# Performance work log

Measured on AMD Instinct MI355X. Metric: run time of the kernel, lower is better.

The kernel has to match this reference:

```python
import jax, jax.numpy as jnp
import numpy as np

N, C_IN, C_OUT, T, V, K = 32, 64, 128, 300, 25, 3
EPS = 1e-5


def setup_inputs() -> dict:
    key = jax.random.key(0)
    ks = jax.random.split(key, 10)
    x = jax.random.normal(ks[0], (N, C_IN, T, V), dtype=jnp.float32)
    # fixed adjacency buffer (requires_grad=False in torch) and learned attention mask
    A = jax.random.uniform(ks[1], (K, V, V), dtype=jnp.float32)
    graph_attn = jnp.ones((K, V, V), dtype=jnp.float32)  # nn.init.constant_(1)
    # per-subset 1x1 conv weights/biases, stacked: [K, C_out, C_in]
    Wg = jax.random.normal(ks[2], (K, C_OUT, C_IN), dtype=jnp.float32) * np.sqrt(2.0 / (C_OUT * K))
    bg = jnp.zeros((K, C_OUT), dtype=jnp.float32)
    # main BN affine (torch init: weight=1e-6, bias=0; use small random for a nontrivial test)
    bn_gamma = jax.random.normal(ks[3], (C_OUT,), dtype=jnp.float32) * 0.1 + 1.0
    bn_beta = jax.random.normal(ks[4], (C_OUT,), dtype=jnp.float32) * 0.1
    # residual branch (in != out): 1x1 conv + BN
    Wr = jax.random.normal(ks[5], (C_OUT, C_IN), dtype=jnp.float32) * np.sqrt(2.0 / C_IN)
    br = jnp.zeros((C_OUT,), dtype=jnp.float32)
    rbn_gamma = jax.random.normal(ks[6], (C_OUT,), dtype=jnp.float32) * 0.1 + 1.0
    rbn_beta = jax.random.normal(ks[7], (C_OUT,), dtype=jnp.float32) * 0.1
    return {"x": x, "A": A, "graph_attn": graph_attn, "Wg": Wg, "bg": bg,
            "bn_gamma": bn_gamma, "bn_beta": bn_beta,
            "Wr": Wr, "br": br, "rbn_gamma": rbn_gamma, "rbn_beta": rbn_beta}


def _batchnorm(z, gamma, beta):
    # training-mode BatchNorm2d: biased batch stats over (N, T, V)
    mean = jnp.mean(z, axis=(0, 2, 3), keepdims=True)
    var = jnp.var(z, axis=(0, 2, 3), keepdims=True)
    zhat = (z - mean) * jax.lax.rsqrt(var + EPS)
    return zhat * gamma[None, :, None, None] + beta[None, :, None, None]


def reference(x, A, graph_attn, Wg, bg, bn_gamma, bn_beta, Wr, br, rbn_gamma, rbn_beta):
    Ae = A * graph_attn                                   # [K, V, V]
    # per-subset graph aggregation: (x.view(N, C*T, V) @ Ae[k])  -> [K, N, C, T, V]
    xA = jnp.einsum('nctv,kvw->knctw', x, Ae)
    # per-subset 1x1 conv then sum over subsets; biases sum as well
    hidden = jnp.einsum('knctv,koc->notv', xA, Wg) + jnp.sum(bg, axis=0)[None, :, None, None]
    hidden = _batchnorm(hidden, bn_gamma, bn_beta)
    # residual: 1x1 conv + BN (since in_channels != out_channels)
    res = jnp.einsum('nctv,oc->notv', x, Wr) + br[None, :, None, None]
    res = _batchnorm(res, rbn_gamma, rbn_beta)
    return hidden + res
```

## Files before the change

kernel.cpp:

```cpp
#include <hip/hip_runtime.h>

typedef __attribute__((ext_vector_type(8))) _Float16 half8;
typedef __attribute__((ext_vector_type(4))) _Float16 half4v;
typedef __attribute__((ext_vector_type(4))) float float4v;
typedef float float4u __attribute__((ext_vector_type(4), aligned(4)));
typedef unsigned long long u64;
typedef unsigned int u32;

#define NB   32
#define CIN  64
#define COUT 128
#define TT   300
#define VV   25
#define EPS  1e-5f
#define M_TOT 240000.0f
#define NBLK 1600
#define NTILE 4800

#define WS_WF    0
#define WS_AEF   65536
#define WS_ST    73728
#define WS_CF    75776
#define WS_WF2   77312
#define WS_TRASH 143360
#define WS_HR    1048576
#define WS_PARTP (WS_HR + 137625600)
#define WS_NEED  (WS_PARTP + 3276800)

__device__ __forceinline__ void bar_lds() {
    __builtin_amdgcn_sched_barrier(0);
    asm volatile("s_waitcnt lgkmcnt(0)" ::: "memory");
    __builtin_amdgcn_s_barrier();
    __builtin_amdgcn_sched_barrier(0);
}

__device__ __forceinline__ unsigned short f2h(float f) {
    return __builtin_bit_cast(unsigned short, (_Float16)f);
}
__device__ __forceinline__ float4v mfma16(half8 a, half8 b, float4v c) {
    return __builtin_amdgcn_mfma_f32_16x16x32_f16(a, b, c, 0, 0, 0);
}
__device__ __forceinline__ u32 pk2(float a, float b) {
    return __builtin_bit_cast(u32, __builtin_amdgcn_cvt_pkrtz(a, b));
}
__device__ __forceinline__ int hr_off(int cm, int on) {
    return (cm & 1) ? (2048 + (cm >> 1) * 768 + on * 384)
                    : ((cm >> 1) * 1024 + on * 512);
}

__global__ void prep_kernel(const float* __restrict__ A, const float* __restrict__ ga,
                            const float* __restrict__ Wg, const float* __restrict__ Wr,
                            char* __restrict__ wsb) {
    unsigned short* wf = (unsigned short*)(wsb + WS_WF);
    unsigned short* ae = (unsigned short*)(wsb + WS_AEF);
    float* st = (float*)(wsb + WS_ST);
    int i = blockIdx.x * blockDim.x + threadIdx.x;
    for (; i < 32768 + 4096 + 512; i += gridDim.x * blockDim.x) {
        if (i < 32768) {
            int on = i >> 12, kt = (i >> 9) & 7, l = (i >> 3) & 63, j = i & 7;
            int o = on * 16 + (l & 15);
            int kc = kt * 32 + ((l >> 4) << 3) + j;
            float v = (kc < 192) ? Wg[((kc >> 6) * COUT + o) * CIN + (kc & 63)]
                                 : Wr[o * CIN + (kc - 192)];
            wf[i] = f2h(v);
        } else if (i < 32768 + 4096) {
            int q = i - 32768;
            int k = q >> 10, nt = (q >> 9) & 1, l = (q >> 3) & 63, j = q & 7;
            int v = ((l >> 4) << 3) + j, w = nt * 16 + (l & 15);
            float val = 0.0f;
            if (v < VV && w < VV)
                val = (k < 3) ? A[(k * VV + v) * VV + w] * ga[(k * VV + v) * VV + w]
                              : (v == w ? 1.0f : 0.0f);
            ae[q] = f2h(val);
        } else {
            st[i - 36864] = 0.0f;
        }
    }
}

__global__ __launch_bounds__(256) void red_kernel(const float* __restrict__ part,
                                                  char* __restrict__ wsb) {
    float* st = (float*)(wsb + WS_ST);
    __shared__ float red[4][4];
    const int tid = threadIdx.x, wv = tid >> 6, lane = tid & 63;
    const int i0 = blockIdx.x * 4;
    const int bi = tid >> 2, ii = tid & 3;
    float s = 0.0f;
    for (int b = bi; b < NBLK; b += 64)
        s += part[(size_t)b * 512 + i0 + ii];
    s += __shfl_xor(s, 4);
    s += __shfl_xor(s, 8);
    s += __shfl_xor(s, 16);
    s += __shfl_xor(s, 32);
    if (lane < 4) red[wv][lane] = s;
    __syncthreads();
    if (tid < 4) st[i0 + tid] = red[0][tid] + red[1][tid] + red[2][tid] + red[3][tid];
}

__global__ __launch_bounds__(256) void scale_kernel(
        const float* __restrict__ Wg, const float* __restrict__ Wr,
        const float* __restrict__ g1, const float* __restrict__ b1,
        const float* __restrict__ g2, const float* __restrict__ b2,
        char* __restrict__ wsb, int fillw2) {
    const float* st = (const float*)(wsb + WS_ST);
    float* cf = (float*)(wsb + WS_CF);
    unsigned short* wf2 = (unsigned short*)(wsb + WS_WF2);
    __shared__ float cl[384];
    int tid = threadIdx.x;
    if (tid < 128) {
        int o = tid;
        const float inv_m = 1.0f / M_TOT;
        float mH = st[o] * inv_m,        vH = st[128 + o] * inv_m - mH * mH;
        float mR = st[256 + o] * inv_m,  vR = st[384 + o] * inv_m - mR * mR;
        float scH = g1[o] * rsqrtf(vH + EPS);
        float scR = g2[o] * rsqrtf(vR + EPS);
        float bC  = b1[o] + b2[o] - scH * mH - scR * mR;
        cl[o] = scH; cl[128 + o] = scR; cl[256 + o] = bC;
        if (blockIdx.x == 0) { cf[o] = scH; cf[128 + o] = scR; cf[256 + o] = bC; }
    }
    __syncthreads();
    if (!fillw2) return;
    for (int i = blockIdx.x * 256 + tid; i < 32768; i += gridDim.x * 256) {
        int on = i >> 12, kt = (i >> 9) & 7, l = (i >> 3) & 63, j = i & 7;
        int o = on * 16 + (l & 15);
        int kc = kt * 32 + ((l >> 4) << 3) + j;
        float v = (kc < 192) ? Wg[((kc >> 6) * COUT + o) * CIN + (kc & 63)] * cl[o]
                             : Wr[o * CIN + (kc - 192)] * cl[128 + o];
        wf2[i] = f2h(v);
    }
}

template <int MODE>
__global__ __launch_bounds__(256, 2) void gcn_kernel(
        const float* __restrict__ x, char* __restrict__ wsb, float* __restrict__ out,
        float* __restrict__ part) {
    __shared__ __align__(16) _Float16 xa[64 * 256];
    __shared__ __align__(16) _Float16 xs[2][64][32];
    char* xab = (char*)xa;

    const unsigned short* wf = (const unsigned short*)(wsb + (MODE == 1 ? WS_WF2 : WS_WF));
    const unsigned short* ae = (const unsigned short*)(wsb + WS_AEF);
    const float* cf = (const float*)(wsb + WS_CF);

    const int tid = threadIdx.x, wv = tid >> 6, l = tid & 63;
    const int l15 = l & 15, lq = l >> 4;

    half8 af[2][8];
#pragma unroll
    for (int on = 0; on < 2; ++on)
#pragma unroll
        for (int kt = 0; kt < 8; ++kt)
            af[on][kt] = *(const half8*)&wf[(((wv * 2 + on) * 8 + kt) * 64 + l) * 8];

    half8 aef[4][2];
#pragma unroll
    for (int k = 0; k < 4; ++k)
#pragma unroll
        for (int nt = 0; nt < 2; ++nt)
            aef[k][nt] = *(const half8*)&ae[((k * 2 + nt) * 64 + l) * 8];

    float bC2[2];
    if (MODE == 1) {
#pragma unroll
        for (int on = 0; on < 2; ++on)
            bC2[on] = cf[256 + wv * 32 + on * 16 + l15];
    }

    float sH[2], sH2[2], sR[2], sR2[2];
    if (MODE != 1) {
#pragma unroll
        for (int on = 0; on < 2; ++on) { sH[on] = 0; sH2[on] = 0; sR[on] = 0; sR2[on] = 0; }
    }

    for (int e = tid; e < 896; e += 256) {
        int t = e / 448, r = e % 448;
        xs[t][r / 7][25 + r % 7] = (_Float16)0.0f;
    }

    float4v pre[4];
    auto issue_pre = [&](int n_, int t0_) {
#pragma unroll
        for (int p = 0; p < 4; ++p) {
            int idx = tid + p * 256;
            int c = idx >> 4, i = idx & 15;
            int f0 = i * 4; f0 = f0 > 46 ? 46 : f0;
            const float* g = x + n_ * 480000 + c * 7500 + t0_ * 25 + f0;
            float4u v = *(const float4u*)g;
            pre[p][0] = v[0]; pre[p][1] = v[1]; pre[p][2] = v[2]; pre[p][3] = v[3];
        }
    };
    auto write_xs = [&]() {
#pragma unroll
        for (int p = 0; p < 4; ++p) {
            int idx = tid + p * 256;
            int c = idx >> 4, i = idx & 15;
            int f0 = i * 4; f0 = f0 > 46 ? 46 : f0;
#pragma unroll
            for (int s = 0; s < 4; ++s) {
                int f = f0 + s;
                int tsel = (f >= 25) ? 1 : 0;
                xs[tsel][c][f - tsel * 25] = (_Float16)pre[p][s];
            }
        }
    };

    const int swb = (blockIdx.x & 7) * (NBLK / 8) + (blockIdx.x >> 3);
    const int tile0 = swb * 3;
    { int n0 = tile0 / 150, t00 = (tile0 % 150) * 2; issue_pre(n0, t00); }
    write_xs();

    for (int it = 0; it < 3; ++it) {
        const int tile = tile0 + it;
        const int n = tile / 150, t0 = (tile % 150) * 2;
        bar_lds();

        const bool hn = (it < 2);
        if (hn) { int tl = tile + 1; issue_pre(tl / 150, (tl % 150) * 2); }

#pragma unroll
        for (int t = 0; t < 2; ++t) {
            half8 xf = *(const half8*)&xs[t][wv * 16 + l15][lq * 8];
#pragma unroll
            for (int k = 0; k < 4; ++k)
#pragma unroll
                for (int nt = 0; nt < 2; ++nt) {
                    float4v c4 = {0.0f, 0.0f, 0.0f, 0.0f};
                    c4 = mfma16(xf, aef[k][nt], c4);
                    int col = t * 32 + nt * 16 + l15;
                    int kcb = (k * 64 + wv * 16 + lq * 4) * 2;
                    u64 pk = ((u64)pk2(c4[2], c4[3]) << 32) | pk2(c4[0], c4[1]);
                    *(u64*)(xab + ((col << 9) + (kcb ^ ((col & 7) << 4)))) = pk;
                }
        }
        bar_lds();

        char* hrw = wsb + WS_HR + (size_t)tile * 28672 + wv * 7168;

        float4v acc[4][2];
        if (MODE != 1) {
#pragma unroll
            for (int cm = 0; cm < 4; ++cm)
#pragma unroll
                for (int on = 0; on < 2; ++on) acc[cm][on] = {0.0f, 0.0f, 0.0f, 0.0f};
            __builtin_amdgcn_s_setprio(1);
#pragma unroll
            for (int kt = 0; kt < 6; ++kt)
#pragma unroll
                for (int cm = 0; cm < 4; ++cm) {
                    int col = cm * 16 + l15;
                    half8 bf = *(const half8*)(xab + ((col << 9) +
                                   ((kt * 64 + lq * 16) ^ ((col & 7) << 4))));
                    acc[cm][0] = mfma16(bf, af[0][kt], acc[cm][0]);
                    acc[cm][1] = mfma16(bf, af[1][kt], acc[cm][1]);
                }
            __builtin_amdgcn_s_setprio(0);
#pragma unroll
            for (int cm = 0; cm < 4; ++cm)
#pragma unroll
                for (int on = 0; on < 2; ++on) {
#pragma unroll
                    for (int r = 0; r < 4; ++r) {
                        float h = acc[cm][on][r];
                        sH[on] += h; sH2[on] += h * h;
                    }
                    if (MODE == 2) {
                        u64 p = (u64)pk2(acc[cm][on][0], acc[cm][on][1]) |
                                ((u64)pk2(acc[cm][on][2], acc[cm][on][3]) << 32);
                        char* dst = hrw + hr_off(cm, on) + l * 8;
                        if ((cm & 1) && lq == 3) dst = wsb + WS_TRASH;
                        *(u64*)dst = p;
                    }
                    acc[cm][on] = {0.0f, 0.0f, 0.0f, 0.0f};
                }
            __builtin_amdgcn_s_setprio(1);
#pragma unroll
            for (int kt = 6; kt < 8; ++kt)
#pragma unroll
                for (int cm = 0; cm < 4; ++cm) {
                    int col = cm * 16 + l15;
                    half8 bf = *(const half8*)(xab + ((col << 9) +
                                   ((kt * 64 + lq * 16) ^ ((col & 7) << 4))));
                    acc[cm][0] = mfma16(bf, af[0][kt], acc[cm][0]);
                    acc[cm][1] = mfma16(bf, af[1][kt], acc[cm][1]);
                }
            __builtin_amdgcn_s_setprio(0);
#pragma unroll
            for (int cm = 0; cm < 4; ++cm)
#pragma unroll
                for (int on = 0; on < 2; ++on) {
#pragma unroll
                    for (int r = 0; r < 4; ++r) {
                        float rv = acc[cm][on][r];
                        sR[on] += rv; sR2[on] += rv * rv;
                    }
                    if (MODE == 2) {
                        u64 p = (u64)pk2(acc[cm][on][0], acc[cm][on][1]) |
                                ((u64)pk2(acc[cm][on][2], acc[cm][on][3]) << 32);
                        char* dst = hrw + 3584 + hr_off(cm, on) + l * 8;
                        if ((cm & 1) && lq == 3) dst = wsb + WS_TRASH;
                        *(u64*)dst = p;
                    }
                }
        } else {
#pragma unroll
            for (int cm = 0; cm < 4; ++cm)
#pragma unroll
                for (int on = 0; on < 2; ++on)
#pragma unroll
                    for (int r = 0; r < 4; ++r) acc[cm][on][r] = bC2[on];
            __builtin_amdgcn_s_setprio(1);
#pragma unroll
            for (int kt = 0; kt < 8; ++kt)
#pragma unroll
                for (int cm = 0; cm < 4; ++cm) {
                    int col = cm * 16 + l15;
                    half8 bf = *(const half8*)(xab + ((col << 9) +
                                   ((kt * 64 + lq * 16) ^ ((col & 7) << 4))));
                    acc[cm][0] = mfma16(bf, af[0][kt], acc[cm][0]);
                    acc[cm][1] = mfma16(bf, af[1][kt], acc[cm][1]);
                }
            __builtin_amdgcn_s_setprio(0);
#pragma unroll
            for (int cm = 0; cm < 4; ++cm) {
                int t = t0 + (cm >> 1);
#pragma unroll
                for (int on = 0; on < 2; ++on) {
                    int o = wv * 32 + on * 16 + l15;
                    float* op = out + ((size_t)(n * COUT + o) * TT + t) * VV;
                    if (!(cm & 1)) {
                        *(float4u*)(op + lq * 4) = acc[cm][on];
                    } else if (lq < 2) {
                        *(float4u*)(op + 16 + lq * 4) = acc[cm][on];
                    } else if (lq == 2) {
                        op[24] = acc[cm][on][0];
                    }
                }
            }
        }

        if (hn) write_xs();

        if (it < 2) {
            __builtin_amdgcn_sched_barrier(0);
            if (MODE == 2) asm volatile("s_waitcnt vmcnt(16) lgkmcnt(0)" ::: "memory");
            else           asm volatile("s_waitcnt vmcnt(0) lgkmcnt(0)" ::: "memory");
            __builtin_amdgcn_s_barrier();
            __builtin_amdgcn_sched_barrier(0);
        }
    }

    if (MODE != 1) {
#pragma unroll
        for (int on = 0; on < 2; ++on) {
            sH[on]  += __shfl_xor(sH[on], 16);  sH[on]  += __shfl_xor(sH[on], 32);
            sH2[on] += __shfl_xor(sH2[on], 16); sH2[on] += __shfl_xor(sH2[on], 32);
            sR[on]  += __shfl_xor(sR[on], 16);  sR[on]  += __shfl_xor(sR[on], 32);
            sR2[on] += __shfl_xor(sR2[on], 16); sR2[on] += __shfl_xor(sR2[on], 32);
        }
        if (l < 16) {
            float* pb = part + (size_t)blockIdx.x * 512;
#pragma unroll
            for (int on = 0; on < 2; ++on) {
                int o = wv * 32 + on * 16 + l15;
                pb[o]       = sH[on];
                pb[128 + o] = sH2[on];
                pb[256 + o] = sR[on];
                pb[384 + o] = sR2[on];
            }
        }
    }
}

__global__ __launch_bounds__(256) void bn_apply(const char* __restrict__ wsb,
                                                float* __restrict__ out) {
    __shared__ u64 lds[3584];
    const float* cf = (const float*)(wsb + WS_CF);
    const int tile = blockIdx.x;
    const int n = tile / 150, t0 = (tile % 150) * 2;
    const int tid = threadIdx.x;

    const u64* src = (const u64*)(wsb + WS_HR + (size_t)tile * 28672);
#pragma unroll
    for (int i = 0; i < 14; ++i) lds[tid + i * 256] = src[tid + i * 256];
    __syncthreads();

#pragma unroll
    for (int i = 0; i < 7; ++i) {
        int j2 = tid + i * 256;
        int row = j2 / 7, q = j2 - row * 7;
        int o = row >> 1, t = row & 1;
        int v0 = (q < 6) ? q * 4 : 24;
        int cm = t * 2 + (v0 >> 4);
        int lq = (v0 & 15) >> 2;
        int ll = lq * 16 + (o & 15);
        int wv = o >> 5, on = (o >> 4) & 1;
        int offq = (cm & 1) ? (256 + (cm >> 1) * 96 + on * 48)
                            : ((cm >> 1) * 128 + on * 64);
        u64 h64 = lds[wv * 896 + offq + ll];
        u64 r64 = lds[wv * 896 + 448 + offq + ll];
        half4v h4 = __builtin_bit_cast(half4v, h64);
        half4v r4 = __builtin_bit_cast(half4v, r64);
        float scH = cf[o], scR = cf[128 + o], bC = cf[256 + o];
        float* op = out + ((size_t)(n * COUT + o) * TT + t0 + t) * VV + v0;
        if (q < 6) {
            float4u v;
#pragma unroll
            for (int k = 0; k < 4; ++k)
                v[k] = scH * (float)h4[k] + scR * (float)r4[k] + bC;
            *(float4u*)op = v;
        } else {
            op[0] = scH * (float)h4[0] + scR * (float)r4[0] + bC;
        }
    }
}

extern "C" void kernel_launch(void* const* d_in, const int* in_sizes, int n_in,
                              void* d_out, int out_size, void* d_ws, size_t ws_size,
                              hipStream_t stream) {
    const float* x        = (const float*)d_in[0];
    const float* A        = (const float*)d_in[1];
    const float* ga       = (const float*)d_in[2];
    const float* Wg       = (const float*)d_in[3];
    const float* bn_gamma = (const float*)d_in[5];
    const float* bn_beta  = (const float*)d_in[6];
    const float* Wr       = (const float*)d_in[7];
    const float* rbn_g    = (const float*)d_in[9];
    const float* rbn_b    = (const float*)d_in[10];
    char* wsb  = (char*)d_ws;
    float* out = (float*)d_out;

    const bool primary = ws_size >= (size_t)WS_NEED + 4096;
    float* partP = (float*)(wsb + WS_PARTP);
    float* partF = (float*)(wsb + WS_HR);

    prep_kernel<<<64, 256, 0, stream>>>(A, ga, Wg, Wr, wsb);
    if (primary) {
        gcn_kernel<2><<<NBLK, 256, 0, stream>>>(x, wsb, nullptr, partP);
        red_kernel<<<128, 256, 0, stream>>>(partP, wsb);
        scale_kernel<<<64, 256, 0, stream>>>(Wg, Wr, bn_gamma, bn_beta, rbn_g, rbn_b, wsb, 0);
        bn_apply<<<NTILE, 256, 0, stream>>>(wsb, out);
    } else {
        gcn_kernel<0><<<NBLK, 256, 0, stream>>>(x, wsb, nullptr, partF);
        red_kernel<<<128, 256, 0, stream>>>(partF, wsb);
        scale_kernel<<<64, 256, 0, stream>>>(Wg, Wr, bn_gamma, bn_beta, rbn_g, rbn_b, wsb, 1);
        gcn_kernel<1><<<NBLK, 256, 0, stream>>>(x, wsb, out, partF);
    }
}
```

Baseline: 122.4 us.

## Load x tiles directly into MFMA operand registers, dropping LDS staging

Each lane now loads the x values for its own MFMA A-fragment straight from global memory into registers and packs them to fp16 in place. This replaces the old path that staged x through an LDS buffer, and removes that buffer, its zero padding, the write pass and the explicit waitcnt/barrier at the end of each iteration. The next tile's loads are still issued early to overlap with compute. The trade-off is less coalesced global loads (per-row float4 reads plus a scalar) and more live registers.

```diff
diff --git a/kernel.cpp b/kernel.cpp
--- a/kernel.cpp
+++ b/kernel.cpp
@@ -3,6 +3,7 @@
 typedef __attribute__((ext_vector_type(8))) _Float16 half8;
 typedef __attribute__((ext_vector_type(4))) _Float16 half4v;
 typedef __attribute__((ext_vector_type(4))) float float4v;
+typedef __attribute__((ext_vector_type(4))) unsigned int uint4v;
 typedef float float4u __attribute__((ext_vector_type(4), aligned(4)));
 typedef unsigned long long u64;
 typedef unsigned int u32;
@@ -135,7 +136,6 @@
         const float* __restrict__ x, char* __restrict__ wsb, float* __restrict__ out,
         float* __restrict__ part) {
     __shared__ __align__(16) _Float16 xa[64 * 256];
-    __shared__ __align__(16) _Float16 xs[2][64][32];
     char* xab = (char*)xa;
 
     const unsigned short* wf = (const unsigned short*)(wsb + (MODE == 1 ? WS_WF2 : WS_WF));
@@ -172,65 +172,55 @@
         for (int on = 0; on < 2; ++on) { sH[on] = 0; sH2[on] = 0; sR[on] = 0; sR2[on] = 0; }
     }
 
-    for (int e = tid; e < 896; e += 256) {
-        int t = e / 448, r = e % 448;
-        xs[t][r / 7][25 + r % 7] = (_Float16)0.0f;
-    }
-
-    float4v pre[4];
-    auto issue_pre = [&](int n_, int t0_) {
-#pragma unroll
-        for (int p = 0; p < 4; ++p) {
-            int idx = tid + p * 256;
-            int c = idx >> 4, i = idx & 15;
-            int f0 = i * 4; f0 = f0 > 46 ? 46 : f0;
-            const float* g = x + n_ * 480000 + c * 7500 + t0_ * 25 + f0;
-            float4u v = *(const float4u*)g;
-            pre[p][0] = v[0]; pre[p][1] = v[1]; pre[p][2] = v[2]; pre[p][3] = v[3];
+    const int cRow = wv * 16 + l15;
+    const int va = (lq * 8 > 16) ? 16 : lq * 8;
+    float4u A1[2], A2[2];
+    float Bv[2];
+    auto ld_tile = [&](int n_, int t0_) {
+#pragma unroll
+        for (int t = 0; t < 2; ++t) {
+            const float* base = x + n_ * 480000 + cRow * 7500 + (t0_ + t) * 25;
+            A1[t] = *(const float4u*)(base + va);
+            A2[t] = *(const float4u*)(base + va + 4);
+            Bv[t] = base[24];
         }
     };
-    auto write_xs = [&]() {
-#pragma unroll
-        for (int p = 0; p < 4; ++p) {
-            int idx = tid + p * 256;
-            int c = idx >> 4, i = idx & 15;
-            int f0 = i * 4; f0 = f0 > 46 ? 46 : f0;
-#pragma unroll
-            for (int s = 0; s < 4; ++s) {
-                int f = f0 + s;
-                int tsel = (f >= 25) ? 1 : 0;
-                xs[tsel][c][f - tsel * 25] = (_Float16)pre[p][s];
-            }
-        }
+    auto mk_xf = [&](int t) -> half8 {
+        u32 w0 = pk2(A1[t][0], A1[t][1]), w1 = pk2(A1[t][2], A1[t][3]);
+        u32 w2 = pk2(A2[t][0], A2[t][1]), w3 = pk2(A2[t][2], A2[t][3]);
+        if (lq == 3) { w0 = pk2(Bv[t], 0.0f); w1 = 0; w2 = 0; w3 = 0; }
+        uint4v uw = {w0, w1, w2, w3};
+        return __builtin_bit_cast(half8, uw);
     };
 
     const int swb = (blockIdx.x & 7) * (NBLK / 8) + (blockIdx.x >> 3);
     const int tile0 = swb * 3;
-    { int n0 = tile0 / 150, t00 = (tile0 % 150) * 2; issue_pre(n0, t00); }
-    write_xs();
+    ld_tile(tile0 / 150, (tile0 % 150) * 2);
 
     for (int it = 0; it < 3; ++it) {
         const int tile = tile0 + it;
         const int n = tile / 150, t0 = (tile % 150) * 2;
         bar_lds();
 
-        const bool hn = (it < 2);
-        if (hn) { int tl = tile + 1; issue_pre(tl / 150, (tl % 150) * 2); }
-
-#pragma unroll
-        for (int t = 0; t < 2; ++t) {
-            half8 xf = *(const half8*)&xs[t][wv * 16 + l15][lq * 8];
-#pragma unroll
-            for (int k = 0; k < 4; ++k)
-#pragma unroll
-                for (int nt = 0; nt < 2; ++nt) {
-                    float4v c4 = {0.0f, 0.0f, 0.0f, 0.0f};
-                    c4 = mfma16(xf, aef[k][nt], c4);
-                    int col = t * 32 + nt * 16 + l15;
-                    int kcb = (k * 64 + wv * 16 + lq * 4) * 2;
-                    u64 pk = ((u64)pk2(c4[2], c4[3]) << 32) | pk2(c4[0], c4[1]);
-                    *(u64*)(xab + ((col << 9) + (kcb ^ ((col & 7) << 4)))) = pk;
-                }
+        half8 xf0 = mk_xf(0);
+        half8 xf1 = mk_xf(1);
+        if (it < 2) { int tl = tile + 1; ld_tile(tl / 150, (tl % 150) * 2); }
+
+        {
+            half8 xfs[2] = {xf0, xf1};
+#pragma unroll
+            for (int t = 0; t < 2; ++t)
+#pragma unroll
+                for (int k = 0; k < 4; ++k)
+#pragma unroll
+                    for (int nt = 0; nt < 2; ++nt) {
+                        float4v c4 = {0.0f, 0.0f, 0.0f, 0.0f};
+                        c4 = mfma16(xfs[t], aef[k][nt], c4);
+                        int col = t * 32 + nt * 16 + l15;
+                        int kcb = (k * 64 + wv * 16 + lq * 4) * 2;
+                        u64 pk = ((u64)pk2(c4[2], c4[3]) << 32) | pk2(c4[0], c4[1]);
+                        *(u64*)(xab + ((col << 9) + (kcb ^ ((col & 7) << 4)))) = pk;
+                    }
         }
         bar_lds();
 
@@ -336,16 +326,6 @@
                     }
                 }
             }
-        }
-
-        if (hn) write_xs();
-
-        if (it < 2) {
-            __builtin_amdgcn_sched_barrier(0);
-            if (MODE == 2) asm volatile("s_waitcnt vmcnt(16) lgkmcnt(0)" ::: "memory");
-            else           asm volatile("s_waitcnt vmcnt(0) lgkmcnt(0)" ::: "memory");
-            __builtin_amdgcn_s_barrier();
-            __builtin_amdgcn_sched_barrier(0);
         }
     }
 
```

New measurement: 131.2 us. +7.2%, slower.
